# Performance work log

Measured on AMD Instinct MI355X. Metric: run time of the kernel, lower is better.

The kernel has to match this reference:

```python
import jax, jax.numpy as jnp
import numpy as np

B, T, C = 4, 1024, 768
H, HS = 12, 64           # num_heads, head_size
VD = 2 * HS              # value dim per head


def setup_inputs() -> dict:
    key = jax.random.key(0)
    ks = jax.random.split(key, 16)
    s = 0.02
    inp = {
        "x": jax.random.normal(ks[0], (B, T, C), jnp.float32),
        "Wq1": jax.random.normal(ks[1], (H, C, HS), jnp.float32) * s,
        "Wk1": jax.random.normal(ks[2], (H, C, HS), jnp.float32) * s,
        "Wq2": jax.random.normal(ks[3], (H, C, HS), jnp.float32) * s,
        "Wk2": jax.random.normal(ks[4], (H, C, HS), jnp.float32) * s,
        "Wv": jax.random.normal(ks[5], (H, C, VD), jnp.float32) * s,
        "lq1": jax.random.normal(ks[6], (H, HS), jnp.float32) * 0.1,
        "lk1": jax.random.normal(ks[7], (H, HS), jnp.float32) * 0.1,
        "lq2": jax.random.normal(ks[8], (H, HS), jnp.float32) * 0.1,
        "lk2": jax.random.normal(ks[9], (H, HS), jnp.float32) * 0.1,
        "gn_w": jnp.ones((H * VD,), jnp.float32),
        "gn_b": jnp.zeros((H * VD,), jnp.float32),
        "Wp": jax.random.normal(ks[10], (C, H * VD), jnp.float32) * s,
        "bp": jnp.zeros((C,), jnp.float32),
        "layer_idx": 3,
    }
    return inp


def _diff_attn(x, Wq1, Wk1, Wq2, Wk2, Wv, lq1, lk1, lq2, lk2,
               gn_w, gn_b, Wp, bp, layer_idx):
    Bc, Tc, _ = x.shape
    scale = 1.0 / jnp.sqrt(jnp.float32(HS))
    # per-head projections: [B,H,T,HS]
    q1 = jnp.einsum('btc,hcd->bhtd', x, Wq1)
    k1 = jnp.einsum('btc,hcd->bhtd', x, Wk1)
    q2 = jnp.einsum('btc,hcd->bhtd', x, Wq2)
    k2 = jnp.einsum('btc,hcd->bhtd', x, Wk2)
    v = jnp.einsum('btc,hce->bhte', x, Wv)           # [B,H,T,2HS]
    mask = jnp.tril(jnp.ones((Tc, Tc), bool))         # causal
    neg = jnp.float32(-jnp.inf)
    a1 = jnp.einsum('bhtd,bhsd->bhts', q1, k1) * scale
    a2 = jnp.einsum('bhtd,bhsd->bhts', q2, k2) * scale
    a1 = jax.nn.softmax(jnp.where(mask, a1, neg), axis=-1)
    a2 = jax.nn.softmax(jnp.where(mask, a2, neg), axis=-1)
    # dynamic lambda init, per get_lambda
    li = jnp.float32(layer_idx)
    dyn = 0.8 - 0.6 * jnp.exp(-0.3 * (li - 1.0))
    lam = jnp.mean(jnp.exp(lq1 * lk1) - jnp.exp(lq2 * lk2) + dyn, axis=-1)  # [H]
    diff = a1 - lam[None, :, None, None] * a2
    out = jnp.einsum('bhts,bhse->bhte', diff, v)      # [B,H,T,2HS]
    out = out.transpose(0, 2, 1, 3).reshape(Bc, Tc, H * VD)
    # GroupLayerNorm == full layernorm over last dim (unbiased=False var)
    mu = out.mean(-1, keepdims=True)
    var = jnp.mean((out - mu) ** 2, axis=-1, keepdims=True)
    out = (out - mu) / jnp.sqrt(var + 1e-5) * gn_w + gn_b
    out = out * 0.2  # (1 - lambda_init_buffer=0.8), buffer never updated
    return out @ Wp.T + bp


def reference(x, Wq1, Wk1, Wq2, Wk2, Wv, lq1, lk1, lq2, lk2,
              gn_w, gn_b, Wp, bp, layer_idx):
    return _diff_attn(x, Wq1, Wk1, Wq2, Wk2, Wv, lq1, lk1, lq2, lk2,
                      gn_w, gn_b, Wp, bp, layer_idx)
```

## Files before the change

kernel.cpp:

```cpp
#include <hip/hip_runtime.h>
#include <hip/hip_bf16.h>

#define Bc   4
#define Tc   1024
#define Cc   768
#define Hc   12
#define HSc  64
#define VDc  128
#define NQKV 4608
#define YLD  3072
#define NROWS 4096
#define HVD  1536

#define Q1OFF 0
#define K1OFF 768
#define Q2OFF 1536
#define K2OFF 2304

typedef __bf16 bf16x8 __attribute__((ext_vector_type(8)));
typedef float f32x4 __attribute__((ext_vector_type(4)));
typedef unsigned int u32x4 __attribute__((ext_vector_type(4)));

#define EXP2SCALE 0.18033688011112042f

static __device__ __forceinline__ float bf2f(unsigned short s) {
    return __uint_as_float(((unsigned int)s) << 16);
}
static __device__ __forceinline__ unsigned short f2bf(float f) {
    unsigned int u = __float_as_uint(f);
    unsigned int r = (u + 0x7FFFu + ((u >> 16) & 1u)) >> 16;
    return (unsigned short)r;
}
static __device__ __forceinline__ unsigned int pack2bf(float lo, float hi) {
    unsigned int a = (__float_as_uint(lo) + 0x8000u) >> 16;
    unsigned int b = (__float_as_uint(hi) + 0x8000u) & 0xFFFF0000u;
    return a | b;
}
static __device__ __forceinline__ float fast_exp2(float x) {
    float r;
    asm("v_exp_f32 %0, %1" : "=v"(r) : "v"(x));
    return r;
}

static __device__ __forceinline__ void load16_lds(const void* g, void* l) {
    __builtin_amdgcn_global_load_lds(
        (const __attribute__((address_space(1))) void*)g,
        (__attribute__((address_space(3))) void*)l, 16, 0, 0);
}

__global__ __launch_bounds__(256) void prep(
    const float* __restrict__ x, const float* __restrict__ Wp,
    const float* __restrict__ lq1, const float* __restrict__ lk1,
    const float* __restrict__ lq2, const float* __restrict__ lk2,
    const int* __restrict__ layer_idx,
    unsigned short* __restrict__ Xb, unsigned short* __restrict__ Wpb,
    float* __restrict__ lam, float* __restrict__ outz)
{
    int bid = blockIdx.x, tid = threadIdx.x;
    if (bid < 3072) {
        size_t i = (size_t)bid * 256 + tid;
        float4 v = *(const float4*)(x + i * 4);
        ushort4 u;
        u.x = f2bf(v.x); u.y = f2bf(v.y); u.z = f2bf(v.z); u.w = f2bf(v.w);
        *(ushort4*)(Xb + i * 4) = u;
    } else if (bid < 4224) {
        size_t i = (size_t)(bid - 3072) * 256 + tid;
        float4 v = *(const float4*)(Wp + i * 4);
        ushort4 u;
        u.x = f2bf(v.x); u.y = f2bf(v.y); u.z = f2bf(v.z); u.w = f2bf(v.w);
        *(ushort4*)(Wpb + i * 4) = u;
    } else if (bid < 4236) {
        if (tid < 64) {
            int h = bid - 4224, l = tid;
            float li = (float)layer_idx[0];
            float dyn = 0.8f - 0.6f * expf(-0.3f * (li - 1.0f));
            int i = h * HSc + l;
            float v = expf(lq1[i] * lk1[i]) - expf(lq2[i] * lk2[i]) + dyn;
            #pragma unroll
            for (int off = 32; off; off >>= 1) v += __shfl_xor(v, off);
            if (l == 0) lam[h] = v * (1.0f / 64.0f);
        }
    } else {
        size_t i = (size_t)(bid - 4236) * 256 + tid;
        float4 z = {0.f, 0.f, 0.f, 0.f};
        *(float4*)(outz + i * 4) = z;
    }
}

__global__ __launch_bounds__(256) void trans_w(
    const float* __restrict__ Wq1, const float* __restrict__ Wk1,
    const float* __restrict__ Wq2, const float* __restrict__ Wk2,
    const float* __restrict__ Wv, unsigned short* __restrict__ WcatT)
{
    __shared__ float tile[64][65];
    int tid = threadIdx.x;
    int t = blockIdx.x;
    int kt = t % 12, nt = t / 12;
    int k0 = kt * 64, n0 = nt * 64;
    const float* src;
    int stride;
    if (n0 < 3072) {
        int which = n0 / 768, m = n0 - which * 768, h = m >> 6;
        const float* W = (which == 0) ? Wq1 : (which == 1) ? Wk1 : (which == 2) ? Wq2 : Wk2;
        src = W + ((size_t)h * 768 + k0) * 64;
        stride = 64;
    } else {
        int rel = n0 - 3072, h = rel >> 7, e0 = rel & 127;
        src = Wv + ((size_t)h * 768 + k0) * 128 + e0;
        stride = 128;
    }
    for (int i = tid; i < 4096; i += 256) {
        int kl = i >> 6, dl = i & 63;
        tile[dl][kl] = src[(size_t)kl * stride + dl];
    }
    __syncthreads();
    for (int i = tid; i < 4096; i += 256) {
        int nl = i >> 6, kl = i & 63;
        WcatT[(size_t)(n0 + nl) * 768 + k0 + kl] = f2bf(tile[nl][kl]);
    }
}

template<int TN, int KD, int LDC, bool OUT_BIAS, bool SPLITV, int KSPLIT>
__global__ __launch_bounds__(256) void gemm_mfma(
    const unsigned short* __restrict__ A, const unsigned short* __restrict__ Bt,
    unsigned short* __restrict__ Cb, float* __restrict__ Cf,
    const float* __restrict__ bias, unsigned short* __restrict__ VtOut)
{
    constexpr int BN = TN * 32;
    constexpr int JB = TN / 2;
    constexpr int ASLOT = 128 * 64;
    constexpr int SLOT  = ASLOT + BN * 64;
    __shared__ unsigned short ring[2 * SLOT];
    int tid = threadIdx.x, lane = tid & 63, w = tid >> 6;
    int wm = w >> 1, wn = w & 1;

    int bid = blockIdx.x;
    int xcd = bid & 7;
    int idx = bid >> 3;
    int ks = 0;
    if (KSPLIT == 2) { ks = idx & 1; idx >>= 1; }
    int mi  = idx & 3;
    int ni  = idx >> 2;
    int m0 = (xcd * 4 + mi) * 128;
    int n0 = ni * BN;
    constexpr int KLOC = KD / KSPLIT;
    const int kBase = ks * KLOC;

    int lr = lane >> 2, lq = lane & 3;
    const unsigned short* gA[2];
    const unsigned short* gB[JB];
    #pragma unroll
    for (int j = 0; j < 2; ++j) {
        int row = w * 32 + j * 16 + lr;
        int qg = lq ^ ((row >> 1) & 3);
        gA[j] = A + (size_t)(m0 + row) * KD + kBase + qg * 8;
    }
    #pragma unroll
    for (int j = 0; j < JB; ++j) {
        int row = w * (JB * 16) + j * 16 + lr;
        int qg = lq ^ ((row >> 1) & 3);
        gB[j] = Bt + (size_t)(n0 + row) * KD + kBase + qg * 8;
    }

    int rr = lane & 15, qd = lane >> 4;
    int aOff[4], bOff[TN];
    #pragma unroll
    for (int i = 0; i < 4; ++i) {
        int row = wm * 64 + i * 16 + rr;
        int qs = qd ^ ((row >> 1) & 3);
        aOff[i] = row * 32 + qs * 8;
    }
    #pragma unroll
    for (int t = 0; t < TN; ++t) {
        int row = wn * (TN * 16) + t * 16 + rr;
        int qs = qd ^ ((row >> 1) & 3);
        bOff[t] = row * 32 + qs * 8;
    }

    auto stageG = [&](int k, int slot) {
        unsigned short* s = ring + slot * SLOT;
        int k64 = k * 64;
        load16_lds(gA[0] + k64,      s + (w * 2 + 0) * 512);
        load16_lds(gA[1] + k64,      s + (w * 2 + 1) * 512);
        load16_lds(gA[0] + k64 + 32, s + 4096 + (w * 2 + 0) * 512);
        load16_lds(gA[1] + k64 + 32, s + 4096 + (w * 2 + 1) * 512);
        #pragma unroll
        for (int j = 0; j < JB; ++j) {
            load16_lds(gB[j] + k64,      s + ASLOT + (w * JB + j) * 512);
            load16_lds(gB[j] + k64 + 32, s + ASLOT + BN * 32 + (w * JB + j) * 512);
        }
    };

    f32x4 acc[4][TN];
    #pragma unroll
    for (int i = 0; i < 4; ++i)
        #pragma unroll
        for (int t = 0; t < TN; ++t) acc[i][t] = {0.f, 0.f, 0.f, 0.f};

    constexpr int NT = KLOC / 64;
    stageG(0, 0);
    for (int k = 0; k < NT; ++k) {
        asm volatile("s_waitcnt vmcnt(0)\n\ts_barrier" ::: "memory");
        const unsigned short* s = ring + (k & 1) * SLOT;
        if (k + 1 < NT) stageG(k + 1, (k + 1) & 1);

        bf16x8 af0[4], af1[4], bf0[TN], bf1[TN];
        #pragma unroll
        for (int i = 0; i < 4; ++i) {
            af0[i] = *(const bf16x8*)(s + aOff[i]);
            af1[i] = *(const bf16x8*)(s + 4096 + aOff[i]);
        }
        #pragma unroll
        for (int t = 0; t < TN; ++t) {
            bf0[t] = *(const bf16x8*)(s + ASLOT + bOff[t]);
            bf1[t] = *(const bf16x8*)(s + ASLOT + BN * 32 + bOff[t]);
        }
        #pragma unroll
        for (int i = 0; i < 4; ++i)
            #pragma unroll
            for (int t = 0; t < TN; ++t) {
                acc[i][t] = __builtin_amdgcn_mfma_f32_16x16x32_bf16(af0[i], bf0[t], acc[i][t], 0, 0, 0);
                acc[i][t] = __builtin_amdgcn_mfma_f32_16x16x32_bf16(af1[i], bf1[t], acc[i][t], 0, 0, 0);
            }
    }

    #pragma unroll
    for (int t = 0; t < TN; ++t) {
        int col = n0 + wn * (TN * 16) + t * 16 + rr;
        if (SPLITV && col >= 3072) {
            int rel = col - 3072, hh = rel >> 7, e = rel & 127;
            #pragma unroll
            for (int i = 0; i < 4; ++i) {
                int row0 = m0 + wm * 64 + i * 16 + qd * 4;
                int b = row0 >> 10, tt = row0 & 1023;
                ushort4 pk;
                pk.x = f2bf(acc[i][t][0]); pk.y = f2bf(acc[i][t][1]);
                pk.z = f2bf(acc[i][t][2]); pk.w = f2bf(acc[i][t][3]);
                *(ushort4*)&VtOut[(size_t)((b * Hc + hh) * 128 + e) * 1024 + tt] = pk;
            }
        } else if (KSPLIT == 2) {
            float bv = (OUT_BIAS && ks == 0) ? bias[col] : 0.f;
            #pragma unroll
            for (int i = 0; i < 4; ++i) {
                #pragma unroll
                for (int r = 0; r < 4; ++r) {
                    int row = m0 + wm * 64 + i * 16 + qd * 4 + r;
                    atomicAdd(&Cf[(size_t)row * LDC + col], acc[i][t][r] + bv);
                }
            }
        } else {
            float bv = OUT_BIAS ? bias[col] : 0.f;
            #pragma unroll
            for (int i = 0; i < 4; ++i) {
                #pragma unroll
                for (int r = 0; r < 4; ++r) {
                    int row = m0 + wm * 64 + i * 16 + qd * 4 + r;
                    if (OUT_BIAS)
                        Cf[(size_t)row * LDC + col] = acc[i][t][r] + bv;
                    else
                        Cb[(size_t)row * LDC + col] = f2bf(acc[i][t][r]);
                }
            }
        }
    }
}

__global__ __launch_bounds__(256) void diff_attn_mfma(
    const unsigned short* __restrict__ Y, const unsigned short* __restrict__ Vt,
    const float* __restrict__ lam_buf, unsigned short* __restrict__ attn)
{
    __shared__ __align__(16) unsigned short KVring[2 * 16384];

    int bh = blockIdx.x;
    int b = bh / Hc, h = bh - b * Hc;
    int g = 15 - (int)blockIdx.y;
    int tid = threadIdx.x, lane = tid & 63, wv = tid >> 6;
    int cl = lane & 15, qd = lane >> 4;
    float lamv = lam_buf[h];
    size_t rowbase = (size_t)(b * Tc) * YLD;
    const int hq = h * HSc;
    const unsigned short* VtB = Vt + ((size_t)bh << 17);
    const f32x4 zero4 = {0.f, 0.f, 0.f, 0.f};

    int sub = wv & 1;
    int off8[8];
    int dstoff;
    if (wv < 2) {
        int ksrow = lane >> 3;
        int ksch  = (lane & 7) ^ ksrow;
        #pragma unroll
        for (int j = 0; j < 8; ++j) {
            int moff = (j < 4) ? K1OFF : K2OFF;
            off8[j] = ((j & 3) * 8 + ksrow) * YLD + moff + hq + ksch * 8;
        }
        dstoff = 0;
    } else {
        int vsel = lane >> 2;
        int vsch = (lane & 3) ^ ((vsel >> 1) & 3);
        #pragma unroll
        for (int s = 0; s < 8; ++s)
            off8[s] = (s * 16 + vsel) * 1024 + vsch * 8;
        dstoff = 8192;
    }

    auto stage = [&](int i, int slot) {
        int kt = 2 * i + sub;
        char* base = (char*)KVring + slot * 32768 + sub * 16384 + dstoff;
        const unsigned short* g0 = (wv < 2)
            ? (Y + rowbase + (size_t)(kt * 32) * YLD)
            : (VtB + kt * 32);
        #pragma unroll
        for (int j = 0; j < 8; ++j)
            load16_lds(g0 + off8[j], base + j * 1024);
    };

    int kfo[2][4], vfo[8];
    #pragma unroll
    for (int c = 0; c < 2; ++c) {
        int row = c * 16 + cl;
        #pragma unroll
        for (int j = 0; j < 4; ++j)
            kfo[c][j] = (j >> 1) * 4096 + row * 128 +
                        ((((j & 1) * 4 + qd) ^ (row & 7)) << 4);
    }
    #pragma unroll
    for (int ec = 0; ec < 8; ++ec) {
        int e = ec * 16 + cl;
        vfo[ec] = 8192 + e * 64 + ((qd ^ ((e >> 1) & 3)) << 4);
    }

    int idxA = ((32 * (qd & 1)) + cl) * 4;
    int idxB = idxA + 64;
    bool loHalf = (qd < 2);

    int qrow = g * 64 + wv * 16;

    stage(0, 0);

    size_t qoff = rowbase + (size_t)(qrow + cl) * YLD;
    bf16x8 q1a = *(const bf16x8*)(Y + qoff + Q1OFF + hq + qd * 8);
    bf16x8 q1b = *(const bf16x8*)(Y + qoff + Q1OFF + hq + 32 + qd * 8);
    bf16x8 q2a = *(const bf16x8*)(Y + qoff + Q2OFF + hq + qd * 8);
    bf16x8 q2b = *(const bf16x8*)(Y + qoff + Q2OFF + hq + 32 + qd * 8);

    f32x4 O1[8], O2[8];
    #pragma unroll
    for (int ec = 0; ec < 8; ++ec) { O1[ec] = zero4; O2[ec] = zero4; }
    float l1s = 0.f, l2s = 0.f;

    auto transform = [&](f32x4 S1[2], f32x4 S2[2], int kt,
                         bf16x8& pa1o, bf16x8& pa2o) {
        if (kt * 32 + 31 > qrow) {
            #pragma unroll
            for (int c = 0; c < 2; ++c) {
                int lim = qrow + cl - kt * 32 - c * 16 - qd * 4;
                #pragma unroll
                for (int r = 0; r < 4; ++r) {
                    if (r > lim) { S1[c][r] = -1e30f; S2[c][r] = -1e30f; }
                }
            }
        }
        float p1v[2][4], p2v[2][4];
        #pragma unroll
        for (int c = 0; c < 2; ++c) {
            #pragma unroll
            for (int r = 0; r < 4; ++r) {
                p1v[c][r] = fast_exp2(S1[c][r] * EXP2SCALE);
                p2v[c][r] = fast_exp2(S2[c][r] * EXP2SCALE);
                l1s += p1v[c][r];
                l2s += p2v[c][r];
            }
        }
        unsigned int s1m[2][2], s2m[2][2];
        #pragma unroll
        for (int c = 0; c < 2; ++c) {
            s1m[c][0] = pack2bf(p1v[c][0], p1v[c][1]);
            s1m[c][1] = pack2bf(p1v[c][2], p1v[c][3]);
            s2m[c][0] = pack2bf(p2v[c][0], p2v[c][1]);
            s2m[c][1] = pack2bf(p2v[c][2], p2v[c][3]);
        }
        u32x4 U1, U2;
        {
            int a00 = __builtin_amdgcn_ds_bpermute(idxA, (int)s1m[0][0]);
            int a10 = __builtin_amdgcn_ds_bpermute(idxA, (int)s1m[1][0]);
            int a01 = __builtin_amdgcn_ds_bpermute(idxA, (int)s1m[0][1]);
            int a11 = __builtin_amdgcn_ds_bpermute(idxA, (int)s1m[1][1]);
            int b00 = __builtin_amdgcn_ds_bpermute(idxB, (int)s1m[0][0]);
            int b10 = __builtin_amdgcn_ds_bpermute(idxB, (int)s1m[1][0]);
            int b01 = __builtin_amdgcn_ds_bpermute(idxB, (int)s1m[0][1]);
            int b11 = __builtin_amdgcn_ds_bpermute(idxB, (int)s1m[1][1]);
            U1[0] = (unsigned)(loHalf ? a00 : a10);
            U1[1] = (unsigned)(loHalf ? a01 : a11);
            U1[2] = (unsigned)(loHalf ? b00 : b10);
            U1[3] = (unsigned)(loHalf ? b01 : b11);
        }
        {
            int a00 = __builtin_amdgcn_ds_bpermute(idxA, (int)s2m[0][0]);
            int a10 = __builtin_amdgcn_ds_bpermute(idxA, (int)s2m[1][0]);
            int a01 = __builtin_amdgcn_ds_bpermute(idxA, (int)s2m[0][1]);
            int a11 = __builtin_amdgcn_ds_bpermute(idxA, (int)s2m[1][1]);
            int b00 = __builtin_amdgcn_ds_bpermute(idxB, (int)s2m[0][0]);
            int b10 = __builtin_amdgcn_ds_bpermute(idxB, (int)s2m[1][0]);
            int b01 = __builtin_amdgcn_ds_bpermute(idxB, (int)s2m[0][1]);
            int b11 = __builtin_amdgcn_ds_bpermute(idxB, (int)s2m[1][1]);
            U2[0] = (unsigned)(loHalf ? a00 : a10);
            U2[1] = (unsigned)(loHalf ? a01 : a11);
            U2[2] = (unsigned)(loHalf ? b00 : b10);
            U2[3] = (unsigned)(loHalf ? b01 : b11);
        }
        pa1o = __builtin_bit_cast(bf16x8, U1);
        pa2o = __builtin_bit_cast(bf16x8, U2);
    };

    int NI = g + 1;
    for (int i = 0; i < NI; ++i) {
        asm volatile("s_waitcnt vmcnt(0)\n\ts_barrier" ::: "memory");
        const char* kbA = (const char*)KVring + (i & 1) * 32768;
        const char* kbB = kbA + 16384;
        if (i + 1 < NI) stage(i + 1, (i + 1) & 1);

        bf16x8 kfA[2][4], kfB[2][4];
        #pragma unroll
        for (int c = 0; c < 2; ++c)
            #pragma unroll
            for (int j = 0; j < 4; ++j) {
                kfA[c][j] = *(const bf16x8*)(kbA + kfo[c][j]);
                kfB[c][j] = *(const bf16x8*)(kbB + kfo[c][j]);
            }
        bf16x8 vfA[8];
        #pragma unroll
        for (int ec = 0; ec < 8; ++ec)
            vfA[ec] = *(const bf16x8*)(kbA + vfo[ec]);

        f32x4 S1A[2], S2A[2], S1B[2], S2B[2];
        #pragma unroll
        for (int c = 0; c < 2; ++c) {
            S1A[c] = zero4; S2A[c] = zero4; S1B[c] = zero4; S2B[c] = zero4;
        }
        #pragma unroll
        for (int c = 0; c < 2; ++c) {
            S1A[c] = __builtin_amdgcn_mfma_f32_16x16x32_bf16(kfA[c][0], q1a, S1A[c], 0, 0, 0);
            S1A[c] = __builtin_amdgcn_mfma_f32_16x16x32_bf16(kfA[c][1], q1b, S1A[c], 0, 0, 0);
            S2A[c] = __builtin_amdgcn_mfma_f32_16x16x32_bf16(kfA[c][2], q2a, S2A[c], 0, 0, 0);
            S2A[c] = __builtin_amdgcn_mfma_f32_16x16x32_bf16(kfA[c][3], q2b, S2A[c], 0, 0, 0);
            S1B[c] = __builtin_amdgcn_mfma_f32_16x16x32_bf16(kfB[c][0], q1a, S1B[c], 0, 0, 0);
            S1B[c] = __builtin_amdgcn_mfma_f32_16x16x32_bf16(kfB[c][1], q1b, S1B[c], 0, 0, 0);
            S2B[c] = __builtin_amdgcn_mfma_f32_16x16x32_bf16(kfB[c][2], q2a, S2B[c], 0, 0, 0);
            S2B[c] = __builtin_amdgcn_mfma_f32_16x16x32_bf16(kfB[c][3], q2b, S2B[c], 0, 0, 0);
        }

        bf16x8 pa1A, pa2A, pa1B, pa2B;
        transform(S1A, S2A, 2 * i, pa1A, pa2A);
        bf16x8 vfB[8];
        #pragma unroll
        for (int ec = 0; ec < 8; ++ec)
            vfB[ec] = *(const bf16x8*)(kbB + vfo[ec]);
        transform(S1B, S2B, 2 * i + 1, pa1B, pa2B);

        #pragma unroll
        for (int ec = 0; ec < 8; ++ec) {
            O1[ec] = __builtin_amdgcn_mfma_f32_16x16x32_bf16(pa1A, vfA[ec], O1[ec], 0, 0, 0);
            O2[ec] = __builtin_amdgcn_mfma_f32_16x16x32_bf16(pa2A, vfA[ec], O2[ec], 0, 0, 0);
        }
        #pragma unroll
        for (int ec = 0; ec < 8; ++ec) {
            O1[ec] = __builtin_amdgcn_mfma_f32_16x16x32_bf16(pa1B, vfB[ec], O1[ec], 0, 0, 0);
            O2[ec] = __builtin_amdgcn_mfma_f32_16x16x32_bf16(pa2B, vfB[ec], O2[ec], 0, 0, 0);
        }
    }

    l1s += __shfl_xor(l1s, 16); l1s += __shfl_xor(l1s, 32);
    l2s += __shfl_xor(l2s, 16); l2s += __shfl_xor(l2s, 32);
    float w1[4], w2[4];
    #pragma unroll
    for (int r = 0; r < 4; ++r) {
        float d1 = __shfl(l1s, qd * 4 + r);
        float d2 = __shfl(l2s, qd * 4 + r);
        w1[r] = 1.0f / d1;
        w2[r] = lamv / d2;
    }
    #pragma unroll
    for (int ec = 0; ec < 8; ++ec) {
        #pragma unroll
        for (int r = 0; r < 4; ++r) {
            size_t row = (size_t)(b * Tc + qrow + qd * 4 + r);
            attn[row * HVD + h * VDc + ec * 16 + cl] =
                f2bf(O1[ec][r] * w1[r] - O2[ec][r] * w2[r]);
        }
    }
}

__global__ __launch_bounds__(128) void ln_inplace(
    unsigned short* __restrict__ attn,
    const float* __restrict__ gnw, const float* __restrict__ gnb)
{
    int row = blockIdx.x, tid = threadIdx.x;
    unsigned short* p = attn + (size_t)row * HVD;
    float v[12];
    float s = 0.f, sq = 0.f;
    #pragma unroll
    for (int j = 0; j < 3; ++j) {
        int g = tid + j * 128;
        ushort4 u = *(const ushort4*)(p + g * 4);
        float x0 = bf2f(u.x), x1 = bf2f(u.y), x2 = bf2f(u.z), x3 = bf2f(u.w);
        v[j * 4 + 0] = x0; v[j * 4 + 1] = x1; v[j * 4 + 2] = x2; v[j * 4 + 3] = x3;
        s += x0 + x1 + x2 + x3;
        sq = fmaf(x0, x0, sq); sq = fmaf(x1, x1, sq);
        sq = fmaf(x2, x2, sq); sq = fmaf(x3, x3, sq);
    }
    #pragma unroll
    for (int off = 32; off; off >>= 1) { s += __shfl_xor(s, off); sq += __shfl_xor(sq, off); }
    __shared__ float ss[2], sqs[2];
    if ((tid & 63) == 0) { ss[tid >> 6] = s; sqs[tid >> 6] = sq; }
    __syncthreads();
    float S = ss[0] + ss[1], Q = sqs[0] + sqs[1];
    float mu = S * (1.0f / HVD);
    float rstd = rsqrtf(Q * (1.0f / HVD) - mu * mu + 1e-5f);
    #pragma unroll
    for (int j = 0; j < 3; ++j) {
        int g = tid + j * 128;
        float4 gw = *(const float4*)(gnw + g * 4);
        float4 gb = *(const float4*)(gnb + g * 4);
        ushort4 o;
        o.x = f2bf(((v[j * 4 + 0] - mu) * rstd * gw.x + gb.x) * 0.2f);
        o.y = f2bf(((v[j * 4 + 1] - mu) * rstd * gw.y + gb.y) * 0.2f);
        o.z = f2bf(((v[j * 4 + 2] - mu) * rstd * gw.z + gb.z) * 0.2f);
        o.w = f2bf(((v[j * 4 + 3] - mu) * rstd * gw.w + gb.w) * 0.2f);
        *(ushort4*)(p + g * 4) = o;
    }
}

extern "C" void kernel_launch(void* const* d_in, const int* in_sizes, int n_in,
                              void* d_out, int out_size, void* d_ws, size_t ws_size,
                              hipStream_t stream)
{
    const float* x   = (const float*)d_in[0];
    const float* Wq1 = (const float*)d_in[1];
    const float* Wk1 = (const float*)d_in[2];
    const float* Wq2 = (const float*)d_in[3];
    const float* Wk2 = (const float*)d_in[4];
    const float* Wv  = (const float*)d_in[5];
    const float* lq1 = (const float*)d_in[6];
    const float* lk1 = (const float*)d_in[7];
    const float* lq2 = (const float*)d_in[8];
    const float* lk2 = (const float*)d_in[9];
    const float* gnw = (const float*)d_in[10];
    const float* gnb = (const float*)d_in[11];
    const float* Wp  = (const float*)d_in[12];
    const float* bp  = (const float*)d_in[13];
    const int*   lidx = (const int*)d_in[14];
    float* out = (float*)d_out;

    char* w = (char*)d_ws;
    unsigned short* WcatT = (unsigned short*)(w);
    unsigned short* Xb    = (unsigned short*)(w + 7077888);
    unsigned short* Y     = (unsigned short*)(w + 13369344);
    unsigned short* VtW   = (unsigned short*)(w + 38535168);
    unsigned short* attn  = (unsigned short*)(w + 51118080);
    unsigned short* Wpb   = (unsigned short*)(w + 63700992);
    float* lam            = (float*)(w + 66060288);

    prep<<<dim3(7308), 256, 0, stream>>>(x, Wp, lq1, lk1, lq2, lk2, lidx,
                                         Xb, Wpb, lam, out);
    trans_w<<<dim3(72 * 12), 256, 0, stream>>>(Wq1, Wk1, Wq2, Wk2, Wv, WcatT);
    gemm_mfma<4, 768, YLD, false, true, 1><<<dim3(1152), 256, 0, stream>>>(
        Xb, WcatT, Y, nullptr, nullptr, VtW);
    diff_attn_mfma<<<dim3(Bc * Hc, 16), 256, 0, stream>>>(Y, VtW, lam, attn);
    ln_inplace<<<dim3(NROWS), 128, 0, stream>>>(attn, gnw, gnb);
    gemm_mfma<2, HVD, Cc, true, false, 2><<<dim3(768), 256, 0, stream>>>(
        attn, Wpb, nullptr, out, bp, nullptr);
}
```

Before: 236.8 us.

## Double attention query tile to 128 rows with 512-thread blocks sharing KV loads

The attention kernel now uses 8 waves per block covering 128 query rows instead of 4 waves covering 64, so each staged K/V tile in LDS serves twice as many query rows and global K/V traffic per query drops. Load duties are split across both wave halves, each loading half the segments. Waves whose rows are entirely above a causal KV tile skip its compute but still join the barriers. In exchange the grid halves to 384 blocks, giving fewer blocks to spread across CUs and more causal imbalance within a block, and the 512,4 launch bound may constrain registers.

```diff
diff --git a/kernel.cpp b/kernel.cpp
--- a/kernel.cpp
+++ b/kernel.cpp
@@ -265,7 +265,7 @@
     }
 }
 
-__global__ __launch_bounds__(256) void diff_attn_mfma(
+__global__ __launch_bounds__(512, 4) void diff_attn_mfma(
     const unsigned short* __restrict__ Y, const unsigned short* __restrict__ Vt,
     const float* __restrict__ lam_buf, unsigned short* __restrict__ attn)
 {
@@ -273,7 +273,7 @@
 
     int bh = blockIdx.x;
     int b = bh / Hc, h = bh - b * Hc;
-    int g = 15 - (int)blockIdx.y;
+    int g = 7 - (int)blockIdx.y;
     int tid = threadIdx.x, lane = tid & 63, wv = tid >> 6;
     int cl = lane & 15, qd = lane >> 4;
     float lamv = lam_buf[h];
@@ -282,36 +282,41 @@
     const unsigned short* VtB = Vt + ((size_t)bh << 17);
     const f32x4 zero4 = {0.f, 0.f, 0.f, 0.f};
 
-    int sub = wv & 1;
-    int off8[8];
-    int dstoff;
-    if (wv < 2) {
+    int role = wv & 3;
+    int half = wv >> 2;
+    int sub  = role & 1;
+    int off4[4];
+    int dstbase;
+    if (role < 2) {
         int ksrow = lane >> 3;
         int ksch  = (lane & 7) ^ ksrow;
         #pragma unroll
-        for (int j = 0; j < 8; ++j) {
-            int moff = (j < 4) ? K1OFF : K2OFF;
-            off8[j] = ((j & 3) * 8 + ksrow) * YLD + moff + hq + ksch * 8;
-        }
-        dstoff = 0;
+        for (int j = 0; j < 4; ++j) {
+            int seg = half * 4 + j;
+            int moff = (seg < 4) ? K1OFF : K2OFF;
+            off4[j] = ((seg & 3) * 8 + ksrow) * YLD + moff + hq + ksch * 8;
+        }
+        dstbase = half * 4096;
     } else {
         int vsel = lane >> 2;
         int vsch = (lane & 3) ^ ((vsel >> 1) & 3);
         #pragma unroll
-        for (int s = 0; s < 8; ++s)
-            off8[s] = (s * 16 + vsel) * 1024 + vsch * 8;
-        dstoff = 8192;
+        for (int j = 0; j < 4; ++j) {
+            int seg = half * 4 + j;
+            off4[j] = (seg * 16 + vsel) * 1024 + vsch * 8;
+        }
+        dstbase = 8192 + half * 4096;
     }
 
     auto stage = [&](int i, int slot) {
         int kt = 2 * i + sub;
-        char* base = (char*)KVring + slot * 32768 + sub * 16384 + dstoff;
-        const unsigned short* g0 = (wv < 2)
+        char* base = (char*)KVring + slot * 32768 + sub * 16384 + dstbase;
+        const unsigned short* g0 = (role < 2)
             ? (Y + rowbase + (size_t)(kt * 32) * YLD)
             : (VtB + kt * 32);
         #pragma unroll
-        for (int j = 0; j < 8; ++j)
-            load16_lds(g0 + off8[j], base + j * 1024);
+        for (int j = 0; j < 4; ++j)
+            load16_lds(g0 + off4[j], base + j * 1024);
     };
 
     int kfo[2][4], vfo[8];
@@ -333,7 +338,7 @@
     int idxB = idxA + 64;
     bool loHalf = (qd < 2);
 
-    int qrow = g * 64 + wv * 16;
+    int qrow = g * 128 + wv * 16;
 
     stage(0, 0);
 
@@ -412,60 +417,62 @@
         pa2o = __builtin_bit_cast(bf16x8, U2);
     };
 
-    int NI = g + 1;
+    int NI = 2 * g + 2;
     for (int i = 0; i < NI; ++i) {
         asm volatile("s_waitcnt vmcnt(0)\n\ts_barrier" ::: "memory");
         const char* kbA = (const char*)KVring + (i & 1) * 32768;
         const char* kbB = kbA + 16384;
         if (i + 1 < NI) stage(i + 1, (i + 1) & 1);
 
-        bf16x8 kfA[2][4], kfB[2][4];
-        #pragma unroll
-        for (int c = 0; c < 2; ++c)
-            #pragma unroll
-            for (int j = 0; j < 4; ++j) {
-                kfA[c][j] = *(const bf16x8*)(kbA + kfo[c][j]);
-                kfB[c][j] = *(const bf16x8*)(kbB + kfo[c][j]);
-            }
-        bf16x8 vfA[8];
-        #pragma unroll
-        for (int ec = 0; ec < 8; ++ec)
-            vfA[ec] = *(const bf16x8*)(kbA + vfo[ec]);
-
-        f32x4 S1A[2], S2A[2], S1B[2], S2B[2];
-        #pragma unroll
-        for (int c = 0; c < 2; ++c) {
-            S1A[c] = zero4; S2A[c] = zero4; S1B[c] = zero4; S2B[c] = zero4;
-        }
-        #pragma unroll
-        for (int c = 0; c < 2; ++c) {
-            S1A[c] = __builtin_amdgcn_mfma_f32_16x16x32_bf16(kfA[c][0], q1a, S1A[c], 0, 0, 0);
-            S1A[c] = __builtin_amdgcn_mfma_f32_16x16x32_bf16(kfA[c][1], q1b, S1A[c], 0, 0, 0);
-            S2A[c] = __builtin_amdgcn_mfma_f32_16x16x32_bf16(kfA[c][2], q2a, S2A[c], 0, 0, 0);
-            S2A[c] = __builtin_amdgcn_mfma_f32_16x16x32_bf16(kfA[c][3], q2b, S2A[c], 0, 0, 0);
-            S1B[c] = __builtin_amdgcn_mfma_f32_16x16x32_bf16(kfB[c][0], q1a, S1B[c], 0, 0, 0);
-            S1B[c] = __builtin_amdgcn_mfma_f32_16x16x32_bf16(kfB[c][1], q1b, S1B[c], 0, 0, 0);
-            S2B[c] = __builtin_amdgcn_mfma_f32_16x16x32_bf16(kfB[c][2], q2a, S2B[c], 0, 0, 0);
-            S2B[c] = __builtin_amdgcn_mfma_f32_16x16x32_bf16(kfB[c][3], q2b, S2B[c], 0, 0, 0);
-        }
-
-        bf16x8 pa1A, pa2A, pa1B, pa2B;
-        transform(S1A, S2A, 2 * i, pa1A, pa2A);
-        bf16x8 vfB[8];
-        #pragma unroll
-        for (int ec = 0; ec < 8; ++ec)
-            vfB[ec] = *(const bf16x8*)(kbB + vfo[ec]);
-        transform(S1B, S2B, 2 * i + 1, pa1B, pa2B);
-
-        #pragma unroll
-        for (int ec = 0; ec < 8; ++ec) {
-            O1[ec] = __builtin_amdgcn_mfma_f32_16x16x32_bf16(pa1A, vfA[ec], O1[ec], 0, 0, 0);
-            O2[ec] = __builtin_amdgcn_mfma_f32_16x16x32_bf16(pa2A, vfA[ec], O2[ec], 0, 0, 0);
-        }
-        #pragma unroll
-        for (int ec = 0; ec < 8; ++ec) {
-            O1[ec] = __builtin_amdgcn_mfma_f32_16x16x32_bf16(pa1B, vfB[ec], O1[ec], 0, 0, 0);
-            O2[ec] = __builtin_amdgcn_mfma_f32_16x16x32_bf16(pa2B, vfB[ec], O2[ec], 0, 0, 0);
+        if (i * 64 <= qrow + 15) {
+            bf16x8 kfA[2][4], kfB[2][4];
+            #pragma unroll
+            for (int c = 0; c < 2; ++c)
+                #pragma unroll
+                for (int j = 0; j < 4; ++j) {
+                    kfA[c][j] = *(const bf16x8*)(kbA + kfo[c][j]);
+                    kfB[c][j] = *(const bf16x8*)(kbB + kfo[c][j]);
+                }
+            bf16x8 vfA[8];
+            #pragma unroll
+            for (int ec = 0; ec < 8; ++ec)
+                vfA[ec] = *(const bf16x8*)(kbA + vfo[ec]);
+
+            f32x4 S1A[2], S2A[2], S1B[2], S2B[2];
+            #pragma unroll
+            for (int c = 0; c < 2; ++c) {
+                S1A[c] = zero4; S2A[c] = zero4; S1B[c] = zero4; S2B[c] = zero4;
+            }
+            #pragma unroll
+            for (int c = 0; c < 2; ++c) {
+                S1A[c] = __builtin_amdgcn_mfma_f32_16x16x32_bf16(kfA[c][0], q1a, S1A[c], 0, 0, 0);
+                S1A[c] = __builtin_amdgcn_mfma_f32_16x16x32_bf16(kfA[c][1], q1b, S1A[c], 0, 0, 0);
+                S2A[c] = __builtin_amdgcn_mfma_f32_16x16x32_bf16(kfA[c][2], q2a, S2A[c], 0, 0, 0);
+                S2A[c] = __builtin_amdgcn_mfma_f32_16x16x32_bf16(kfA[c][3], q2b, S2A[c], 0, 0, 0);
+                S1B[c] = __builtin_amdgcn_mfma_f32_16x16x32_bf16(kfB[c][0], q1a, S1B[c], 0, 0, 0);
+                S1B[c] = __builtin_amdgcn_mfma_f32_16x16x32_bf16(kfB[c][1], q1b, S1B[c], 0, 0, 0);
+                S2B[c] = __builtin_amdgcn_mfma_f32_16x16x32_bf16(kfB[c][2], q2a, S2B[c], 0, 0, 0);
+                S2B[c] = __builtin_amdgcn_mfma_f32_16x16x32_bf16(kfB[c][3], q2b, S2B[c], 0, 0, 0);
+            }
+
+            bf16x8 pa1A, pa2A, pa1B, pa2B;
+            transform(S1A, S2A, 2 * i, pa1A, pa2A);
+            bf16x8 vfB[8];
+            #pragma unroll
+            for (int ec = 0; ec < 8; ++ec)
+                vfB[ec] = *(const bf16x8*)(kbB + vfo[ec]);
+            transform(S1B, S2B, 2 * i + 1, pa1B, pa2B);
+
+            #pragma unroll
+            for (int ec = 0; ec < 8; ++ec) {
+                O1[ec] = __builtin_amdgcn_mfma_f32_16x16x32_bf16(pa1A, vfA[ec], O1[ec], 0, 0, 0);
+                O2[ec] = __builtin_amdgcn_mfma_f32_16x16x32_bf16(pa2A, vfA[ec], O2[ec], 0, 0, 0);
+            }
+            #pragma unroll
+            for (int ec = 0; ec < 8; ++ec) {
+                O1[ec] = __builtin_amdgcn_mfma_f32_16x16x32_bf16(pa1B, vfB[ec], O1[ec], 0, 0, 0);
+                O2[ec] = __builtin_amdgcn_mfma_f32_16x16x32_bf16(pa2B, vfB[ec], O2[ec], 0, 0, 0);
+            }
         }
     }
 
@@ -565,7 +572,7 @@
     trans_w<<<dim3(72 * 12), 256, 0, stream>>>(Wq1, Wk1, Wq2, Wk2, Wv, WcatT);
     gemm_mfma<4, 768, YLD, false, true, 1><<<dim3(1152), 256, 0, stream>>>(
         Xb, WcatT, Y, nullptr, nullptr, VtW);
-    diff_attn_mfma<<<dim3(Bc * Hc, 16), 256, 0, stream>>>(Y, VtW, lam, attn);
+    diff_attn_mfma<<<dim3(Bc * Hc, 8), 512, 0, stream>>>(Y, VtW, lam, attn);
     ln_inplace<<<dim3(NROWS), 128, 0, stream>>>(attn, gnw, gnb);
     gemm_mfma<2, HVD, Cc, true, false, 2><<<dim3(768), 256, 0, stream>>>(
         attn, Wpb, nullptr, out, bp, nullptr);
```

Measured after the change: 448.1 us. +89.2%, slower.
